# Optimization experiments

Hardware: AMD Instinct MI355X
Metric: run time of the kernel (lower is better)

The kernel has to match this reference:

```python
import jax, jax.numpy as jnp
import numpy as np

B = 1024      # batch
DIN = 103     # generator/encoder input dim
L1, L2 = 64, 32   # encoder layer widths (latent = 32)
E = 8         # NUM_EXPERTS
GH = 64       # gating hidden width
H = 256       # generator hidden width
DOUT = 51     # generator output dim
EPS = 1e-5    # BatchNorm eps


def setup_inputs() -> dict:
    key = jax.random.key(0)
    ks = jax.random.split(key, 24)
    s = 0.05
    f32 = jnp.float32
    return {
        "x": jax.random.normal(ks[0], (B, DIN), f32),
        # encoder Linear + BN params
        "w1": jax.random.normal(ks[1], (L1, DIN), f32) * s,
        "b1": jnp.zeros((L1,), f32),
        "gamma1": jnp.ones((L1,), f32),
        "beta1": jnp.zeros((L1,), f32),
        "w2": jax.random.normal(ks[2], (L2, L1), f32) * s,
        "b2": jnp.zeros((L2,), f32),
        "gamma2": jnp.ones((L2,), f32),
        "beta2": jnp.zeros((L2,), f32),
        # gating MLP (latent 32 -> GH -> GH -> E, ELU, softmax)
        "gw1": jax.random.normal(ks[3], (GH, L2), f32) * s,
        "gb1": jnp.zeros((GH,), f32),
        "gw2": jax.random.normal(ks[4], (GH, GH), f32) * s,
        "gb2": jnp.zeros((GH,), f32),
        "gw3": jax.random.normal(ks[5], (E, GH), f32) * s,
        "gb3": jnp.zeros((E,), f32),
        # expert weight banks for 3-layer generator (MANN style)
        "ew1": jax.random.normal(ks[6], (E, DIN, H), f32) * s,
        "eb1": jnp.zeros((E, H), f32),
        "ew2": jax.random.normal(ks[7], (E, H, H), f32) * s,
        "eb2": jnp.zeros((E, H), f32),
        "ew3": jax.random.normal(ks[8], (E, H, DOUT), f32) * s,
        "eb3": jnp.zeros((E, DOUT), f32),
    }


def _batchnorm(h, gamma, beta):
    # training-mode BatchNorm1d: per-batch mean/var (biased var, matching torch)
    m = jnp.mean(h, axis=0)
    v = jnp.mean((h - m) ** 2, axis=0)
    return gamma * (h - m) * jax.lax.rsqrt(v + EPS) + beta


def reference(x, w1, b1, gamma1, beta1, w2, b2, gamma2, beta2,
              gw1, gb1, gw2, gb2, gw3, gb3,
              ew1, eb1, ew2, eb2, ew3, eb3):
    # in-place scale of last 3 features (x[:,100:103] *= 100)
    xs = x.at[:, 100:103].multiply(100.0)
    # encoder: Linear -> BN -> ReLU, twice
    h = jax.nn.relu(_batchnorm(xs @ w1.T + b1, gamma1, beta1))
    latent = jax.nn.relu(_batchnorm(h @ w2.T + b2, gamma2, beta2))
    # gating network -> blending coefficients BC [B, E]
    g = jax.nn.elu(latent @ gw1.T + gb1)
    g = jax.nn.elu(g @ gw2.T + gb2)
    bc = jax.nn.softmax(g @ gw3.T + gb3, axis=-1)
    # MANN-style generator: per-sample expert-blended weights
    wb1 = jnp.einsum('be,eih->bih', bc, ew1)   # [B, DIN, H]
    h1 = jax.nn.elu(jnp.einsum('bi,bih->bh', xs, wb1) + bc @ eb1)
    wb2 = jnp.einsum('be,ehk->bhk', bc, ew2)   # [B, H, H]
    h2 = jax.nn.elu(jnp.einsum('bh,bhk->bk', h1, wb2) + bc @ eb2)
    wb3 = jnp.einsum('be,eho->bho', bc, ew3)   # [B, H, DOUT]
    out = jnp.einsum('bh,bho->bo', h2, wb3) + bc @ eb3
    return out
```

## Files before the change

### kernel.cpp

```cpp
#include <hip/hip_runtime.h>
#include <math.h>


#define DIN 103
#define NE  8
#define HH  256
#define DOUT 51
#define EPSBN 1e-5f

typedef __attribute__((ext_vector_type(8))) short bf16x8;
typedef __attribute__((ext_vector_type(4))) float f32x4;
typedef __attribute__((ext_vector_type(8))) unsigned short us8;
typedef unsigned short ushort_t;

__device__ __forceinline__ float eluf(float v) { return v > 0.f ? v : (expf(v) - 1.f); }
__device__ __forceinline__ unsigned short bf16h(float f) {
  unsigned u = __float_as_uint(f);
  u += 0x7FFFu + ((u >> 16) & 1u);
  return (unsigned short)(u >> 16);
}
__device__ __forceinline__ float bf16f(unsigned short h) { return __uint_as_float(((unsigned)h) << 16); }
__device__ __forceinline__ void split_bf16(float v, unsigned short& h, unsigned short& l) {
  h = bf16h(v);
  l = bf16h(v - bf16f(h));
}
#define MFMA __builtin_amdgcn_mfma_f32_16x16x32_bf16

#define O_SLOTS1 0
#define O_SLOTS2 8192
#define O_BCG    12288
#define O_H1RAW  20480
#define O_H2RAW  86016
#define O_XSH    118784
#define O_XSL    184320
#define O_W1H    249856
#define O_W1L    253952
#define O_E1H    258048
#define O_E1L    389120
#define O_E2H    520192
#define O_E3H    782336
#define O_A1H    847872
#define O_A1L    978944
#define O_A2H    1110016
#define O_A2L    1241088
#define O_P      1372160

__global__ __launch_bounds__(256) void k_prep(
    const float* __restrict__ x, const float* __restrict__ w1,
    const float* __restrict__ ew1, const float* __restrict__ ew2, const float* __restrict__ ew3,
    float* __restrict__ ws) {
  __shared__ float tile[32][65];
  int bk = blockIdx.x, t = threadIdx.x;
  int l2 = t & 63, c = l2 & 15, q = l2 >> 4;

  if (bk < 256) {
    int nh = bk & 3, kc = (bk >> 2) & 7, e = bk >> 5;
    int k0 = kc * 32, n0 = nh * 64;
#pragma unroll
    for (int i = 0; i < 8; ++i) {
      int kl = (t >> 6) + i * 4;
      tile[kl][t & 63] = ew2[((size_t)e * HH + k0 + kl) * HH + n0 + (t & 63)];
    }
    __syncthreads();
    int nsl = t >> 6;
    us8 H8;
#pragma unroll
    for (int j = 0; j < 8; ++j) H8[j] = bf16h(tile[q * 8 + j][nsl * 16 + c]);
    size_t dst = (((size_t)(e * 16 + nh * 4 + nsl)) * 8 + kc) * 512 + l2 * 8;
    *(us8*)((ushort_t*)(ws + O_E2H) + dst) = H8;
  } else if (bk < 384) {
    int b2 = bk - 256;
    int nh = b2 & 3, kc = (b2 >> 2) & 3, e = b2 >> 4;
    int k0 = kc * 32, n0 = nh * 64;
#pragma unroll
    for (int i = 0; i < 8; ++i) {
      int kl = (t >> 6) + i * 4;
      int k = k0 + kl;
      tile[kl][t & 63] = (k < DIN) ? ew1[((size_t)e * DIN + k) * HH + n0 + (t & 63)] : 0.f;
    }
    __syncthreads();
    int nsl = t >> 6;
    us8 H8, L8;
#pragma unroll
    for (int j = 0; j < 8; ++j) {
      unsigned short h, lo; split_bf16(tile[q * 8 + j][nsl * 16 + c], h, lo);
      H8[j] = h; L8[j] = lo;
    }
    size_t dst = (((size_t)(e * 16 + nh * 4 + nsl)) * 4 + kc) * 512 + l2 * 8;
    *(us8*)((ushort_t*)(ws + O_E1H) + dst) = H8;
    *(us8*)((ushort_t*)(ws + O_E1L) + dst) = L8;
  } else if (bk < 448) {
    int b2 = bk - 384;
    int kc = b2 & 7, e = b2 >> 3;
    int k0 = kc * 32;
#pragma unroll
    for (int i = 0; i < 8; ++i) {
      int kl = (t >> 6) + i * 4;
      int n = t & 63;
      tile[kl][n] = (n < DOUT) ? ew3[((size_t)e * HH + k0 + kl) * DOUT + n] : 0.f;
    }
    __syncthreads();
    int nsl = t >> 6;
    us8 H8;
#pragma unroll
    for (int j = 0; j < 8; ++j) H8[j] = bf16h(tile[q * 8 + j][nsl * 16 + c]);
    size_t dst = (((size_t)(e * 4 + nsl)) * 8 + kc) * 512 + l2 * 8;
    *(us8*)((ushort_t*)(ws + O_E3H) + dst) = H8;
  } else if (bk < 452) {
    int kc = bk - 448;
    int k0 = kc * 32;
    __shared__ float tw[64][33];
#pragma unroll
    for (int p8 = 0; p8 < 8; ++p8) {
      int j = (t >> 5) + p8 * 8;
      int kl = t & 31;
      int k = k0 + kl;
      tw[j][kl] = (k < DIN) ? w1[(size_t)j * DIN + k] : 0.f;
    }
    __syncthreads();
    int nsl = t >> 6;
    us8 H8, L8;
#pragma unroll
    for (int j = 0; j < 8; ++j) {
      unsigned short h, lo; split_bf16(tw[nsl * 16 + c][q * 8 + j], h, lo);
      H8[j] = h; L8[j] = lo;
    }
    size_t dst = ((size_t)nsl * 4 + kc) * 512 + l2 * 8;
    *(us8*)((ushort_t*)(ws + O_W1H) + dst) = H8;
    *(us8*)((ushort_t*)(ws + O_W1L) + dst) = L8;
  } else {
    int msub = bk - 452;
    __shared__ float xt[16][104];
    for (int i = t; i < 16 * 104; i += 256) {
      int b = i / 104, k = i - b * 104;
      float v = 0.f;
      if (k < DIN) { v = x[(size_t)(msub * 16 + b) * DIN + k]; if (k >= 100) v *= 100.f; }
      xt[b][k] = v;
    }
    __syncthreads();
    int kc = t >> 6;
    int m = c;
    us8 H8, L8;
#pragma unroll
    for (int j = 0; j < 8; ++j) {
      int k = kc * 32 + q * 8 + j;
      float v = (k < 104) ? xt[m][k] : 0.f;
      unsigned short h, lo; split_bf16(v, h, lo);
      H8[j] = h; L8[j] = lo;
    }
    size_t dst = ((size_t)msub * 4 + kc) * 512 + l2 * 8;
    *(us8*)((ushort_t*)(ws + O_XSH) + dst) = H8;
    *(us8*)((ushort_t*)(ws + O_XSL) + dst) = L8;
  }
}

__global__ __launch_bounds__(256) void k_enc1(const float* __restrict__ b1, float* __restrict__ ws) {
  __shared__ float tile[16][65];
  int bk = blockIdx.x, t = threadIdx.x;
  int wv = t >> 6, l = t & 63, c = l & 15, quad = l >> 4;
  const ushort_t* XsH = (const ushort_t*)(ws + O_XSH);
  const ushort_t* XsL = (const ushort_t*)(ws + O_XSL);
  const ushort_t* W1H = (const ushort_t*)(ws + O_W1H);
  const ushort_t* W1L = (const ushort_t*)(ws + O_W1L);
  float* h1raw  = ws + O_H1RAW;
  float* slots1 = ws + O_SLOTS1;
  f32x4 acc = {0.f, 0.f, 0.f, 0.f};
#pragma unroll
  for (int kc = 0; kc < 4; ++kc) {
    bf16x8 ah = *(const bf16x8*)(XsH + ((size_t)bk * 4 + kc) * 512 + l * 8);
    bf16x8 al = *(const bf16x8*)(XsL + ((size_t)bk * 4 + kc) * 512 + l * 8);
    bf16x8 bh = *(const bf16x8*)(W1H + ((size_t)wv * 4 + kc) * 512 + l * 8);
    bf16x8 bl = *(const bf16x8*)(W1L + ((size_t)wv * 4 + kc) * 512 + l * 8);
    acc = MFMA(ah, bh, acc, 0, 0, 0);
    acc = MFMA(al, bh, acc, 0, 0, 0);
    acc = MFMA(ah, bl, acc, 0, 0, 0);
  }
  int col = wv * 16 + c;
  float b1v = b1[col];
#pragma unroll
  for (int r = 0; r < 4; ++r) {
    float v = acc[r] + b1v;
    tile[quad * 4 + r][col] = v;
    h1raw[(size_t)(bk * 16 + quad * 4 + r) * 64 + col] = v;
  }
  __syncthreads();
  if (t < 64) {
    float s = 0.f, qq = 0.f;
    for (int r = 0; r < 16; ++r) { float v = tile[r][t]; s += v; qq += v * v; }
    slots1[bk * 128 + t] = s;
    slots1[bk * 128 + 64 + t] = qq;
  }
}

__global__ __launch_bounds__(256) void k_enc2(
    const float* __restrict__ gamma1, const float* __restrict__ beta1,
    const float* __restrict__ w2, const float* __restrict__ b2, float* __restrict__ ws) {
  __shared__ float w2T[64 * 33];
  __shared__ float red[128];
  __shared__ float sc1[64], sh1[64];
  __shared__ float h1b[16][64];
  __shared__ float hb2[16][32];
  float* slots1 = ws + O_SLOTS1;
  float* slots2 = ws + O_SLOTS2;
  float* h1raw  = ws + O_H1RAW;
  float* h2raw  = ws + O_H2RAW;
  int bk = blockIdx.x, t = threadIdx.x;
  int R0 = bk * 16;
  for (int i = t; i < 2048; i += 256) { int j = i >> 6, k = i & 63; w2T[k * 33 + j] = w2[i]; }
  if (t < 128) {
    float s = 0.f;
    for (int b = 0; b < 64; ++b) s += slots1[b * 128 + t];
    red[t] = s;
  }
  __syncthreads();
  if (t < 64) {
    float m = red[t] * (1.f / 1024.f);
    float v = red[64 + t] * (1.f / 1024.f) - m * m;
    float sc = gamma1[t] * rsqrtf(v + EPSBN);
    sc1[t] = sc; sh1[t] = beta1[t] - m * sc;
  }
  __syncthreads();
#pragma unroll
  for (int i = 0; i < 4; ++i) {
    int idx = t + i * 256;
    int r = idx >> 6, k = idx & 63;
    h1b[r][k] = fmaxf(fmaf(h1raw[(size_t)(R0 + r) * 64 + k], sc1[k], sh1[k]), 0.f);
  }
  __syncthreads();
#pragma unroll
  for (int i = 0; i < 2; ++i) {
    int o = t + i * 256;
    int r = o >> 5, j = o & 31;
    float acc = b2[j];
    for (int k = 0; k < 64; ++k) acc = fmaf(h1b[r][k], w2T[k * 33 + j], acc);
    hb2[r][j] = acc;
    h2raw[(size_t)(R0 + r) * 32 + j] = acc;
  }
  __syncthreads();
  if (t < 32) {
    float s = 0.f, q = 0.f;
    for (int r = 0; r < 16; ++r) { float v = hb2[r][t]; s += v; q += v * v; }
    slots2[bk * 64 + t] = s;
    slots2[bk * 64 + 32 + t] = q;
  }
}

__global__ __launch_bounds__(256) void k_gate(
    const float* __restrict__ gamma2, const float* __restrict__ beta2,
    const float* __restrict__ gw1, const float* __restrict__ gb1,
    const float* __restrict__ gw2, const float* __restrict__ gb2,
    const float* __restrict__ gw3, const float* __restrict__ gb3,
    float* __restrict__ ws) {
  __shared__ float red2[64], sc2[32], sh2[32];
  __shared__ float lat[16][32];
  __shared__ float gw1L[64 * 33], gw2L[64 * 65], gw3L[8 * 65];
  __shared__ float gb1L[64], gb2L[64], gb3L[8];
  __shared__ float g1[16][64], g2[16][64];
  float* slots2 = ws + O_SLOTS2;
  float* bcg    = ws + O_BCG;
  float* h2raw  = ws + O_H2RAW;
  int bk = blockIdx.x, t = threadIdx.x;
  int wv = t >> 6, l = t & 63;
  int R0 = bk * 16;
  for (int i = t; i < 2048; i += 256) { int j = i >> 5, k = i & 31; gw1L[j * 33 + k] = gw1[i]; }
  for (int i = t; i < 4096; i += 256) { int j = i >> 6, k = i & 63; gw2L[j * 65 + k] = gw2[i]; }
  for (int i = t; i < 512; i += 256) { int j = i >> 6, k = i & 63; gw3L[j * 65 + k] = gw3[i]; }
  if (t < 64) { gb1L[t] = gb1[t]; gb2L[t] = gb2[t]; }
  if (t < 8) gb3L[t] = gb3[t];
  if (t < 64) {
    float s = 0.f;
    for (int b = 0; b < 64; ++b) s += slots2[b * 64 + t];
    red2[t] = s;
  }
  __syncthreads();
  if (t < 32) {
    float m = red2[t] * (1.f / 1024.f);
    float v = red2[32 + t] * (1.f / 1024.f) - m * m;
    float sc = gamma2[t] * rsqrtf(v + EPSBN);
    sc2[t] = sc; sh2[t] = beta2[t] - m * sc;
  }
  __syncthreads();
#pragma unroll
  for (int i = 0; i < 2; ++i) {
    int idx = t + i * 256;
    int r = idx >> 5, cc = idx & 31;
    lat[r][cc] = fmaxf(fmaf(h2raw[(size_t)(R0 + r) * 32 + cc], sc2[cc], sh2[cc]), 0.f);
  }
  __syncthreads();
#pragma unroll
  for (int rr = 0; rr < 4; ++rr) {
    int r = wv * 4 + rr;
    float a1 = gb1L[l];
    for (int k = 0; k < 32; ++k) a1 = fmaf(gw1L[l * 33 + k], lat[r][k], a1);
    g1[r][l] = eluf(a1);
  }
  __syncthreads();
#pragma unroll
  for (int rr = 0; rr < 4; ++rr) {
    int r = wv * 4 + rr;
    float a2 = gb2L[l];
    for (int k = 0; k < 64; ++k) a2 = fmaf(gw2L[l * 65 + k], g1[r][k], a2);
    g2[r][l] = eluf(a2);
  }
  __syncthreads();
#pragma unroll
  for (int rr = 0; rr < 4; ++rr) {
    int r = wv * 4 + rr;
    if (l < 8) {
      float a3 = gb3L[l];
      for (int k = 0; k < 64; ++k) a3 = fmaf(gw3L[l * 65 + k], g2[r][k], a3);
      float mx = a3;
      mx = fmaxf(mx, __shfl_xor(mx, 1));
      mx = fmaxf(mx, __shfl_xor(mx, 2));
      mx = fmaxf(mx, __shfl_xor(mx, 4));
      float p = expf(a3 - mx);
      float sp = p;
      sp += __shfl_xor(sp, 1); sp += __shfl_xor(sp, 2); sp += __shfl_xor(sp, 4);
      bcg[(size_t)(R0 + r) * 8 + l] = p / sp;
    }
  }
}

__global__ __launch_bounds__(256) void k_gen1(float* __restrict__ ws) {
  int bk = blockIdx.x, e = blockIdx.y, t = threadIdx.x;
  int wv = t >> 6, l = t & 63, c = l & 15, quad = l >> 4;
  const ushort_t* XsH = (const ushort_t*)(ws + O_XSH);
  const ushort_t* XsL = (const ushort_t*)(ws + O_XSL);
  const ushort_t* E1H = (const ushort_t*)(ws + O_E1H);
  const ushort_t* E1L = (const ushort_t*)(ws + O_E1L);
  float* p = ws + O_P;
  f32x4 acc[4] = {};
#pragma unroll
  for (int kc = 0; kc < 4; ++kc) {
    bf16x8 ah = *(const bf16x8*)(XsH + ((size_t)bk * 4 + kc) * 512 + l * 8);
    bf16x8 al = *(const bf16x8*)(XsL + ((size_t)bk * 4 + kc) * 512 + l * 8);
#pragma unroll
    for (int nsi = 0; nsi < 4; ++nsi) {
      int ns = wv * 4 + nsi;
      size_t bo = (((size_t)(e * 16 + ns)) * 4 + kc) * 512 + l * 8;
      bf16x8 bh = *(const bf16x8*)(E1H + bo);
      bf16x8 bl = *(const bf16x8*)(E1L + bo);
      acc[nsi] = MFMA(ah, bh, acc[nsi], 0, 0, 0);
      acc[nsi] = MFMA(al, bh, acc[nsi], 0, 0, 0);
      acc[nsi] = MFMA(ah, bl, acc[nsi], 0, 0, 0);
    }
  }
  float* pe = p + (size_t)e * 262144;
#pragma unroll
  for (int nsi = 0; nsi < 4; ++nsi) {
    int col = (wv * 4 + nsi) * 16 + c;
#pragma unroll
    for (int r = 0; r < 4; ++r)
      pe[(size_t)(bk * 16 + quad * 4 + r) * 256 + col] = acc[nsi][r];
  }
}

__global__ __launch_bounds__(256) void k_gen2(float* __restrict__ ws) {
  int bk = blockIdx.x, e = blockIdx.y, t = threadIdx.x;
  int wv = t >> 6, l = t & 63, c = l & 15, quad = l >> 4;
  const ushort_t* AH = (const ushort_t*)(ws + O_A1H);
  const ushort_t* AL = (const ushort_t*)(ws + O_A1L);
  const ushort_t* E2H = (const ushort_t*)(ws + O_E2H);
  float* p = ws + O_P;
  f32x4 acc[4] = {};
#pragma unroll
  for (int kc = 0; kc < 8; ++kc) {
    bf16x8 ah = *(const bf16x8*)(AH + ((size_t)bk * 8 + kc) * 512 + l * 8);
    bf16x8 al = *(const bf16x8*)(AL + ((size_t)bk * 8 + kc) * 512 + l * 8);
#pragma unroll
    for (int nsi = 0; nsi < 4; ++nsi) {
      int ns = wv * 4 + nsi;
      size_t bo = (((size_t)(e * 16 + ns)) * 8 + kc) * 512 + l * 8;
      bf16x8 bh = *(const bf16x8*)(E2H + bo);
      acc[nsi] = MFMA(ah, bh, acc[nsi], 0, 0, 0);
      acc[nsi] = MFMA(al, bh, acc[nsi], 0, 0, 0);
    }
  }
  float* pe = p + (size_t)e * 262144;
#pragma unroll
  for (int nsi = 0; nsi < 4; ++nsi) {
    int col = (wv * 4 + nsi) * 16 + c;
#pragma unroll
    for (int r = 0; r < 4; ++r)
      pe[(size_t)(bk * 16 + quad * 4 + r) * 256 + col] = acc[nsi][r];
  }
}

__global__ __launch_bounds__(256) void k_gen3(float* __restrict__ ws) {
  int bk = blockIdx.x, eg = blockIdx.y, t = threadIdx.x;
  int wv = t >> 6, l = t & 63, c = l & 15, quad = l >> 4;
  int e = eg * 4 + wv;
  const ushort_t* AH = (const ushort_t*)(ws + O_A2H);
  const ushort_t* AL = (const ushort_t*)(ws + O_A2L);
  const ushort_t* E3H = (const ushort_t*)(ws + O_E3H);
  float* p3 = ws + O_P;
  f32x4 acc[4] = {};
#pragma unroll
  for (int kc = 0; kc < 8; ++kc) {
    bf16x8 ah = *(const bf16x8*)(AH + ((size_t)bk * 8 + kc) * 512 + l * 8);
    bf16x8 al = *(const bf16x8*)(AL + ((size_t)bk * 8 + kc) * 512 + l * 8);
#pragma unroll
    for (int nsi = 0; nsi < 4; ++nsi) {
      size_t bo = (((size_t)(e * 4 + nsi)) * 8 + kc) * 512 + l * 8;
      bf16x8 bh = *(const bf16x8*)(E3H + bo);
      acc[nsi] = MFMA(ah, bh, acc[nsi], 0, 0, 0);
      acc[nsi] = MFMA(al, bh, acc[nsi], 0, 0, 0);
    }
  }
  float* pe = p3 + (size_t)e * 65536;
#pragma unroll
  for (int nsi = 0; nsi < 4; ++nsi) {
    int col = nsi * 16 + c;
#pragma unroll
    for (int r = 0; r < 4; ++r)
      pe[(size_t)(bk * 16 + quad * 4 + r) * 64 + col] = acc[nsi][r];
  }
}

__global__ __launch_bounds__(256) void k_comb(const float* __restrict__ eb,
    float* __restrict__ ws, int dstH, int dstL) {
  int gid = blockIdx.x * 256 + threadIdx.x;
  int l2 = gid & 63, kc = (gid >> 6) & 7, msub = gid >> 9;
  int b = msub * 16 + (l2 & 15);
  int k0 = kc * 32 + (l2 >> 4) * 8;
  const float* p = ws + O_P;
  const float* bc = ws + O_BCG;
  unsigned short* ah = (unsigned short*)(ws + dstH);
  unsigned short* al = (unsigned short*)(ws + dstL);
  float wv[NE];
#pragma unroll
  for (int e = 0; e < NE; ++e) wv[e] = bc[b * NE + e];
  float s[8] = {};
#pragma unroll
  for (int e = 0; e < NE; ++e) {
    const float* pr = p + (size_t)e * 262144 + (size_t)b * HH + k0;
    float4 p0 = *(const float4*)pr, p1 = *(const float4*)(pr + 4);
    const float* er = eb + e * HH + k0;
    float4 e0 = *(const float4*)er, e1 = *(const float4*)(er + 4);
    s[0] = fmaf(wv[e], p0.x + e0.x, s[0]);
    s[1] = fmaf(wv[e], p0.y + e0.y, s[1]);
    s[2] = fmaf(wv[e], p0.z + e0.z, s[2]);
    s[3] = fmaf(wv[e], p0.w + e0.w, s[3]);
    s[4] = fmaf(wv[e], p1.x + e1.x, s[4]);
    s[5] = fmaf(wv[e], p1.y + e1.y, s[5]);
    s[6] = fmaf(wv[e], p1.z + e1.z, s[6]);
    s[7] = fmaf(wv[e], p1.w + e1.w, s[7]);
  }
  us8 H, L;
#pragma unroll
  for (int j = 0; j < 8; ++j) {
    float v = eluf(s[j]);
    unsigned short h, lo; split_bf16(v, h, lo);
    H[j] = h; L[j] = lo;
  }
  *(us8*)(ah + (size_t)gid * 8) = H;
  *(us8*)(al + (size_t)gid * 8) = L;
}

__global__ __launch_bounds__(256) void k_comb3(const float* __restrict__ eb3,
    float* __restrict__ ws, float* __restrict__ out) {
  int gid = blockIdx.x * 256 + threadIdx.x;
  int b = gid >> 6, o = gid & 63;
  if (o >= DOUT) return;
  const float* p3 = ws + O_P;
  const float* bc = ws + O_BCG;
  float s = 0.f;
#pragma unroll
  for (int e = 0; e < NE; ++e)
    s = fmaf(bc[b * NE + e], p3[(size_t)e * 65536 + (size_t)b * 64 + o] + eb3[e * DOUT + o], s);
  out[(size_t)b * DOUT + o] = s;
}

extern "C" void kernel_launch(void* const* d_in, const int* in_sizes, int n_in,
                              void* d_out, int out_size, void* d_ws, size_t ws_size,
                              hipStream_t stream) {
  const float* x      = (const float*)d_in[0];
  const float* w1     = (const float*)d_in[1];
  const float* b1     = (const float*)d_in[2];
  const float* gamma1 = (const float*)d_in[3];
  const float* beta1  = (const float*)d_in[4];
  const float* w2     = (const float*)d_in[5];
  const float* b2     = (const float*)d_in[6];
  const float* gamma2 = (const float*)d_in[7];
  const float* beta2  = (const float*)d_in[8];
  const float* gw1    = (const float*)d_in[9];
  const float* gb1    = (const float*)d_in[10];
  const float* gw2    = (const float*)d_in[11];
  const float* gb2    = (const float*)d_in[12];
  const float* gw3    = (const float*)d_in[13];
  const float* gb3    = (const float*)d_in[14];
  const float* ew1    = (const float*)d_in[15];
  const float* eb1    = (const float*)d_in[16];
  const float* ew2    = (const float*)d_in[17];
  const float* eb2    = (const float*)d_in[18];
  const float* ew3    = (const float*)d_in[19];
  const float* eb3    = (const float*)d_in[20];
  float* wsf  = (float*)d_ws;
  float* outp = (float*)d_out;

  k_prep<<<516, 256, 0, stream>>>(x, w1, ew1, ew2, ew3, wsf);
  k_enc1<<<64, 256, 0, stream>>>(b1, wsf);
  k_enc2<<<64, 256, 0, stream>>>(gamma1, beta1, w2, b2, wsf);
  k_gate<<<64, 256, 0, stream>>>(gamma2, beta2, gw1, gb1, gw2, gb2, gw3, gb3, wsf);
  k_gen1<<<dim3(64, 8), 256, 0, stream>>>(wsf);
  k_comb<<<128, 256, 0, stream>>>(eb1, wsf, O_A1H, O_A1L);
  k_gen2<<<dim3(64, 8), 256, 0, stream>>>(wsf);
  k_comb<<<128, 256, 0, stream>>>(eb2, wsf, O_A2H, O_A2L);
  k_gen3<<<dim3(64, 2), 256, 0, stream>>>(wsf);
  k_comb3<<<256, 256, 0, stream>>>(eb3, wsf, outp);
}
```

Before: 160.1 us.

## Merge independent kernels to cut launches and fuse gen3 with final combine

Merges k_prep with enc1, computing the first encoder layer in plain FP32 from shared memory instead of the MFMA path with split bf16. Runs gen1 and the gating network as disjoint block ranges of a single launch, since they do not depend on each other. Fuses gen3 and comb3 into one 512-thread kernel that keeps per-expert partials in shared memory rather than writing them to global memory. This takes the launch count from 10 to 7 and removes one global round trip, at the cost of larger blocks and a slower scalar enc1.

```diff
diff --git a/kernel.cpp b/kernel.cpp
--- a/kernel.cpp
+++ b/kernel.cpp
@@ -33,8 +33,6 @@
 #define O_H2RAW  86016
 #define O_XSH    118784
 #define O_XSL    184320
-#define O_W1H    249856
-#define O_W1L    253952
 #define O_E1H    258048
 #define O_E1L    389120
 #define O_E2H    520192
@@ -45,11 +43,15 @@
 #define O_A2L    1241088
 #define O_P      1372160
 
-__global__ __launch_bounds__(256) void k_prep(
-    const float* __restrict__ x, const float* __restrict__ w1,
+__global__ __launch_bounds__(256) void k_prep_enc1(
+    const float* __restrict__ x, const float* __restrict__ w1, const float* __restrict__ b1,
     const float* __restrict__ ew1, const float* __restrict__ ew2, const float* __restrict__ ew3,
     float* __restrict__ ws) {
-  __shared__ float tile[32][65];
+  __shared__ union {
+    float tile[32][65];
+    float xt[16][104];
+    struct { float w1L[64 * DIN]; float xr[16][104]; float hb[16][64]; } e1;
+  } sm;
   int bk = blockIdx.x, t = threadIdx.x;
   int l2 = t & 63, c = l2 & 15, q = l2 >> 4;
 
@@ -59,13 +61,13 @@
 #pragma unroll
     for (int i = 0; i < 8; ++i) {
       int kl = (t >> 6) + i * 4;
-      tile[kl][t & 63] = ew2[((size_t)e * HH + k0 + kl) * HH + n0 + (t & 63)];
+      sm.tile[kl][t & 63] = ew2[((size_t)e * HH + k0 + kl) * HH + n0 + (t & 63)];
     }
     __syncthreads();
     int nsl = t >> 6;
     us8 H8;
 #pragma unroll
-    for (int j = 0; j < 8; ++j) H8[j] = bf16h(tile[q * 8 + j][nsl * 16 + c]);
+    for (int j = 0; j < 8; ++j) H8[j] = bf16h(sm.tile[q * 8 + j][nsl * 16 + c]);
     size_t dst = (((size_t)(e * 16 + nh * 4 + nsl)) * 8 + kc) * 512 + l2 * 8;
     *(us8*)((ushort_t*)(ws + O_E2H) + dst) = H8;
   } else if (bk < 384) {
@@ -76,14 +78,14 @@
     for (int i = 0; i < 8; ++i) {
       int kl = (t >> 6) + i * 4;
       int k = k0 + kl;
-      tile[kl][t & 63] = (k < DIN) ? ew1[((size_t)e * DIN + k) * HH + n0 + (t & 63)] : 0.f;
+      sm.tile[kl][t & 63] = (k < DIN) ? ew1[((size_t)e * DIN + k) * HH + n0 + (t & 63)] : 0.f;
     }
     __syncthreads();
     int nsl = t >> 6;
     us8 H8, L8;
 #pragma unroll
     for (int j = 0; j < 8; ++j) {
-      unsigned short h, lo; split_bf16(tile[q * 8 + j][nsl * 16 + c], h, lo);
+      unsigned short h, lo; split_bf16(sm.tile[q * 8 + j][nsl * 16 + c], h, lo);
       H8[j] = h; L8[j] = lo;
     }
     size_t dst = (((size_t)(e * 16 + nh * 4 + nsl)) * 4 + kc) * 512 + l2 * 8;
@@ -97,45 +99,22 @@
     for (int i = 0; i < 8; ++i) {
       int kl = (t >> 6) + i * 4;
       int n = t & 63;
-      tile[kl][n] = (n < DOUT) ? ew3[((size_t)e * HH + k0 + kl) * DOUT + n] : 0.f;
+      sm.tile[kl][n] = (n < DOUT) ? ew3[((size_t)e * HH + k0 + kl) * DOUT + n] : 0.f;
     }
     __syncthreads();
     int nsl = t >> 6;
     us8 H8;
 #pragma unroll
-    for (int j = 0; j < 8; ++j) H8[j] = bf16h(tile[q * 8 + j][nsl * 16 + c]);
+    for (int j = 0; j < 8; ++j) H8[j] = bf16h(sm.tile[q * 8 + j][nsl * 16 + c]);
     size_t dst = (((size_t)(e * 4 + nsl)) * 8 + kc) * 512 + l2 * 8;
     *(us8*)((ushort_t*)(ws + O_E3H) + dst) = H8;
-  } else if (bk < 452) {
-    int kc = bk - 448;
-    int k0 = kc * 32;
-    __shared__ float tw[64][33];
-#pragma unroll
-    for (int p8 = 0; p8 < 8; ++p8) {
-      int j = (t >> 5) + p8 * 8;
-      int kl = t & 31;
-      int k = k0 + kl;
-      tw[j][kl] = (k < DIN) ? w1[(size_t)j * DIN + k] : 0.f;
-    }
-    __syncthreads();
-    int nsl = t >> 6;
-    us8 H8, L8;
-#pragma unroll
-    for (int j = 0; j < 8; ++j) {
-      unsigned short h, lo; split_bf16(tw[nsl * 16 + c][q * 8 + j], h, lo);
-      H8[j] = h; L8[j] = lo;
-    }
-    size_t dst = ((size_t)nsl * 4 + kc) * 512 + l2 * 8;
-    *(us8*)((ushort_t*)(ws + O_W1H) + dst) = H8;
-    *(us8*)((ushort_t*)(ws + O_W1L) + dst) = L8;
-  } else {
-    int msub = bk - 452;
-    __shared__ float xt[16][104];
+  } else if (bk < 512) {
+    int msub = bk - 448;
     for (int i = t; i < 16 * 104; i += 256) {
       int b = i / 104, k = i - b * 104;
       float v = 0.f;
       if (k < DIN) { v = x[(size_t)(msub * 16 + b) * DIN + k]; if (k >= 100) v *= 100.f; }
-      xt[b][k] = v;
+      sm.xt[b][k] = v;
     }
     __syncthreads();
     int kc = t >> 6;
@@ -144,51 +123,42 @@
 #pragma unroll
     for (int j = 0; j < 8; ++j) {
       int k = kc * 32 + q * 8 + j;
-      float v = (k < 104) ? xt[m][k] : 0.f;
+      float v = (k < 104) ? sm.xt[m][k] : 0.f;
       unsigned short h, lo; split_bf16(v, h, lo);
       H8[j] = h; L8[j] = lo;
     }
     size_t dst = ((size_t)msub * 4 + kc) * 512 + l2 * 8;
     *(us8*)((ushort_t*)(ws + O_XSH) + dst) = H8;
     *(us8*)((ushort_t*)(ws + O_XSL) + dst) = L8;
-  }
-}
-
-__global__ __launch_bounds__(256) void k_enc1(const float* __restrict__ b1, float* __restrict__ ws) {
-  __shared__ float tile[16][65];
-  int bk = blockIdx.x, t = threadIdx.x;
-  int wv = t >> 6, l = t & 63, c = l & 15, quad = l >> 4;
-  const ushort_t* XsH = (const ushort_t*)(ws + O_XSH);
-  const ushort_t* XsL = (const ushort_t*)(ws + O_XSL);
-  const ushort_t* W1H = (const ushort_t*)(ws + O_W1H);
-  const ushort_t* W1L = (const ushort_t*)(ws + O_W1L);
-  float* h1raw  = ws + O_H1RAW;
-  float* slots1 = ws + O_SLOTS1;
-  f32x4 acc = {0.f, 0.f, 0.f, 0.f};
-#pragma unroll
-  for (int kc = 0; kc < 4; ++kc) {
-    bf16x8 ah = *(const bf16x8*)(XsH + ((size_t)bk * 4 + kc) * 512 + l * 8);
-    bf16x8 al = *(const bf16x8*)(XsL + ((size_t)bk * 4 + kc) * 512 + l * 8);
-    bf16x8 bh = *(const bf16x8*)(W1H + ((size_t)wv * 4 + kc) * 512 + l * 8);
-    bf16x8 bl = *(const bf16x8*)(W1L + ((size_t)wv * 4 + kc) * 512 + l * 8);
-    acc = MFMA(ah, bh, acc, 0, 0, 0);
-    acc = MFMA(al, bh, acc, 0, 0, 0);
-    acc = MFMA(ah, bl, acc, 0, 0, 0);
-  }
-  int col = wv * 16 + c;
-  float b1v = b1[col];
-#pragma unroll
-  for (int r = 0; r < 4; ++r) {
-    float v = acc[r] + b1v;
-    tile[quad * 4 + r][col] = v;
-    h1raw[(size_t)(bk * 16 + quad * 4 + r) * 64 + col] = v;
-  }
-  __syncthreads();
-  if (t < 64) {
-    float s = 0.f, qq = 0.f;
-    for (int r = 0; r < 16; ++r) { float v = tile[r][t]; s += v; qq += v * v; }
-    slots1[bk * 128 + t] = s;
-    slots1[bk * 128 + 64 + t] = qq;
+  } else {
+    float* slots1 = ws + O_SLOTS1;
+    float* h1raw  = ws + O_H1RAW;
+    int bkl = bk - 512;
+    int r0 = bkl * 16;
+    for (int i = t; i < 64 * DIN; i += 256) sm.e1.w1L[i] = w1[i];
+    for (int i = t; i < 16 * 104; i += 256) {
+      int r = i / 104, c2 = i - r * 104;
+      float v = 0.f;
+      if (c2 < DIN) { v = x[(size_t)(r0 + r) * DIN + c2]; if (c2 >= 100) v *= 100.f; }
+      sm.e1.xr[r][c2] = v;
+    }
+    __syncthreads();
+#pragma unroll
+    for (int i = 0; i < 4; ++i) {
+      int idx = t + i * 256;
+      int r = idx >> 6, j = idx & 63;
+      float acc = b1[j];
+      for (int k = 0; k < DIN; ++k) acc = fmaf(sm.e1.xr[r][k], sm.e1.w1L[j * DIN + k], acc);
+      sm.e1.hb[r][j] = acc;
+      h1raw[(size_t)(r0 + r) * 64 + j] = acc;
+    }
+    __syncthreads();
+    if (t < 64) {
+      float s = 0.f, qq = 0.f;
+      for (int r = 0; r < 16; ++r) { float v = sm.e1.hb[r][t]; s += v; qq += v * v; }
+      slots1[bkl * 128 + t] = s;
+      slots1[bkl * 128 + 64 + t] = qq;
+    }
   }
 }
 
@@ -245,113 +215,114 @@
   }
 }
 
-__global__ __launch_bounds__(256) void k_gate(
+__global__ __launch_bounds__(256) void k_gen1_gate(
     const float* __restrict__ gamma2, const float* __restrict__ beta2,
     const float* __restrict__ gw1, const float* __restrict__ gb1,
     const float* __restrict__ gw2, const float* __restrict__ gb2,
     const float* __restrict__ gw3, const float* __restrict__ gb3,
     float* __restrict__ ws) {
-  __shared__ float red2[64], sc2[32], sh2[32];
-  __shared__ float lat[16][32];
-  __shared__ float gw1L[64 * 33], gw2L[64 * 65], gw3L[8 * 65];
-  __shared__ float gb1L[64], gb2L[64], gb3L[8];
-  __shared__ float g1[16][64], g2[16][64];
-  float* slots2 = ws + O_SLOTS2;
-  float* bcg    = ws + O_BCG;
-  float* h2raw  = ws + O_H2RAW;
-  int bk = blockIdx.x, t = threadIdx.x;
+  int blk = blockIdx.x, t = threadIdx.x;
   int wv = t >> 6, l = t & 63;
-  int R0 = bk * 16;
-  for (int i = t; i < 2048; i += 256) { int j = i >> 5, k = i & 31; gw1L[j * 33 + k] = gw1[i]; }
-  for (int i = t; i < 4096; i += 256) { int j = i >> 6, k = i & 63; gw2L[j * 65 + k] = gw2[i]; }
-  for (int i = t; i < 512; i += 256) { int j = i >> 6, k = i & 63; gw3L[j * 65 + k] = gw3[i]; }
-  if (t < 64) { gb1L[t] = gb1[t]; gb2L[t] = gb2[t]; }
-  if (t < 8) gb3L[t] = gb3[t];
-  if (t < 64) {
-    float s = 0.f;
-    for (int b = 0; b < 64; ++b) s += slots2[b * 64 + t];
-    red2[t] = s;
-  }
-  __syncthreads();
-  if (t < 32) {
-    float m = red2[t] * (1.f / 1024.f);
-    float v = red2[32 + t] * (1.f / 1024.f) - m * m;
-    float sc = gamma2[t] * rsqrtf(v + EPSBN);
-    sc2[t] = sc; sh2[t] = beta2[t] - m * sc;
-  }
-  __syncthreads();
-#pragma unroll
-  for (int i = 0; i < 2; ++i) {
-    int idx = t + i * 256;
-    int r = idx >> 5, cc = idx & 31;
-    lat[r][cc] = fmaxf(fmaf(h2raw[(size_t)(R0 + r) * 32 + cc], sc2[cc], sh2[cc]), 0.f);
-  }
-  __syncthreads();
-#pragma unroll
-  for (int rr = 0; rr < 4; ++rr) {
-    int r = wv * 4 + rr;
-    float a1 = gb1L[l];
-    for (int k = 0; k < 32; ++k) a1 = fmaf(gw1L[l * 33 + k], lat[r][k], a1);
-    g1[r][l] = eluf(a1);
-  }
-  __syncthreads();
-#pragma unroll
-  for (int rr = 0; rr < 4; ++rr) {
-    int r = wv * 4 + rr;
-    float a2 = gb2L[l];
-    for (int k = 0; k < 64; ++k) a2 = fmaf(gw2L[l * 65 + k], g1[r][k], a2);
-    g2[r][l] = eluf(a2);
-  }
-  __syncthreads();
-#pragma unroll
-  for (int rr = 0; rr < 4; ++rr) {
-    int r = wv * 4 + rr;
-    if (l < 8) {
-      float a3 = gb3L[l];
-      for (int k = 0; k < 64; ++k) a3 = fmaf(gw3L[l * 65 + k], g2[r][k], a3);
-      float mx = a3;
-      mx = fmaxf(mx, __shfl_xor(mx, 1));
-      mx = fmaxf(mx, __shfl_xor(mx, 2));
-      mx = fmaxf(mx, __shfl_xor(mx, 4));
-      float p = expf(a3 - mx);
-      float sp = p;
-      sp += __shfl_xor(sp, 1); sp += __shfl_xor(sp, 2); sp += __shfl_xor(sp, 4);
-      bcg[(size_t)(R0 + r) * 8 + l] = p / sp;
-    }
-  }
-}
-
-__global__ __launch_bounds__(256) void k_gen1(float* __restrict__ ws) {
-  int bk = blockIdx.x, e = blockIdx.y, t = threadIdx.x;
-  int wv = t >> 6, l = t & 63, c = l & 15, quad = l >> 4;
-  const ushort_t* XsH = (const ushort_t*)(ws + O_XSH);
-  const ushort_t* XsL = (const ushort_t*)(ws + O_XSL);
-  const ushort_t* E1H = (const ushort_t*)(ws + O_E1H);
-  const ushort_t* E1L = (const ushort_t*)(ws + O_E1L);
-  float* p = ws + O_P;
-  f32x4 acc[4] = {};
-#pragma unroll
-  for (int kc = 0; kc < 4; ++kc) {
-    bf16x8 ah = *(const bf16x8*)(XsH + ((size_t)bk * 4 + kc) * 512 + l * 8);
-    bf16x8 al = *(const bf16x8*)(XsL + ((size_t)bk * 4 + kc) * 512 + l * 8);
+  if (blk < 512) {
+    int bk = blk >> 3, e = blk & 7;
+    int c = l & 15, quad = l >> 4;
+    const ushort_t* XsH = (const ushort_t*)(ws + O_XSH);
+    const ushort_t* XsL = (const ushort_t*)(ws + O_XSL);
+    const ushort_t* E1H = (const ushort_t*)(ws + O_E1H);
+    const ushort_t* E1L = (const ushort_t*)(ws + O_E1L);
+    float* p = ws + O_P;
+    f32x4 acc[4] = {};
+#pragma unroll
+    for (int kc = 0; kc < 4; ++kc) {
+      bf16x8 ah = *(const bf16x8*)(XsH + ((size_t)bk * 4 + kc) * 512 + l * 8);
+      bf16x8 al = *(const bf16x8*)(XsL + ((size_t)bk * 4 + kc) * 512 + l * 8);
+#pragma unroll
+      for (int nsi = 0; nsi < 4; ++nsi) {
+        int ns = wv * 4 + nsi;
+        size_t bo = (((size_t)(e * 16 + ns)) * 4 + kc) * 512 + l * 8;
+        bf16x8 bh = *(const bf16x8*)(E1H + bo);
+        bf16x8 bl = *(const bf16x8*)(E1L + bo);
+        acc[nsi] = MFMA(ah, bh, acc[nsi], 0, 0, 0);
+        acc[nsi] = MFMA(al, bh, acc[nsi], 0, 0, 0);
+        acc[nsi] = MFMA(ah, bl, acc[nsi], 0, 0, 0);
+      }
+    }
+    float* pe = p + (size_t)e * 262144;
 #pragma unroll
     for (int nsi = 0; nsi < 4; ++nsi) {
-      int ns = wv * 4 + nsi;
-      size_t bo = (((size_t)(e * 16 + ns)) * 4 + kc) * 512 + l * 8;
-      bf16x8 bh = *(const bf16x8*)(E1H + bo);
-      bf16x8 bl = *(const bf16x8*)(E1L + bo);
-      acc[nsi] = MFMA(ah, bh, acc[nsi], 0, 0, 0);
-      acc[nsi] = MFMA(al, bh, acc[nsi], 0, 0, 0);
-      acc[nsi] = MFMA(ah, bl, acc[nsi], 0, 0, 0);
-    }
-  }
-  float* pe = p + (size_t)e * 262144;
-#pragma unroll
-  for (int nsi = 0; nsi < 4; ++nsi) {
-    int col = (wv * 4 + nsi) * 16 + c;
-#pragma unroll
-    for (int r = 0; r < 4; ++r)
-      pe[(size_t)(bk * 16 + quad * 4 + r) * 256 + col] = acc[nsi][r];
+      int col = (wv * 4 + nsi) * 16 + c;
+#pragma unroll
+      for (int r = 0; r < 4; ++r)
+        pe[(size_t)(bk * 16 + quad * 4 + r) * 256 + col] = acc[nsi][r];
+    }
+  } else {
+    __shared__ float red2[64], sc2[32], sh2[32];
+    __shared__ float lat[16][32];
+    __shared__ float gw1L[64 * 33], gw2L[64 * 65], gw3L[8 * 65];
+    __shared__ float gb1L[64], gb2L[64], gb3L[8];
+    __shared__ float g1[16][64], g2[16][64];
+    float* slots2 = ws + O_SLOTS2;
+    float* bcg    = ws + O_BCG;
+    float* h2raw  = ws + O_H2RAW;
+    int bk = blk - 512;
+    int R0 = bk * 16;
+    for (int i = t; i < 2048; i += 256) { int j = i >> 5, k = i & 31; gw1L[j * 33 + k] = gw1[i]; }
+    for (int i = t; i < 4096; i += 256) { int j = i >> 6, k = i & 63; gw2L[j * 65 + k] = gw2[i]; }
+    for (int i = t; i < 512; i += 256) { int j = i >> 6, k = i & 63; gw3L[j * 65 + k] = gw3[i]; }
+    if (t < 64) { gb1L[t] = gb1[t]; gb2L[t] = gb2[t]; }
+    if (t < 8) gb3L[t] = gb3[t];
+    if (t < 64) {
+      float s = 0.f;
+      for (int b = 0; b < 64; ++b) s += slots2[b * 64 + t];
+      red2[t] = s;
+    }
+    __syncthreads();
+    if (t < 32) {
+      float m = red2[t] * (1.f / 1024.f);
+      float v = red2[32 + t] * (1.f / 1024.f) - m * m;
+      float sc = gamma2[t] * rsqrtf(v + EPSBN);
+      sc2[t] = sc; sh2[t] = beta2[t] - m * sc;
+    }
+    __syncthreads();
+#pragma unroll
+    for (int i = 0; i < 2; ++i) {
+      int idx = t + i * 256;
+      int r = idx >> 5, cc = idx & 31;
+      lat[r][cc] = fmaxf(fmaf(h2raw[(size_t)(R0 + r) * 32 + cc], sc2[cc], sh2[cc]), 0.f);
+    }
+    __syncthreads();
+#pragma unroll
+    for (int rr = 0; rr < 4; ++rr) {
+      int r = wv * 4 + rr;
+      float a1 = gb1L[l];
+      for (int k = 0; k < 32; ++k) a1 = fmaf(gw1L[l * 33 + k], lat[r][k], a1);
+      g1[r][l] = eluf(a1);
+    }
+    __syncthreads();
+#pragma unroll
+    for (int rr = 0; rr < 4; ++rr) {
+      int r = wv * 4 + rr;
+      float a2 = gb2L[l];
+      for (int k = 0; k < 64; ++k) a2 = fmaf(gw2L[l * 65 + k], g1[r][k], a2);
+      g2[r][l] = eluf(a2);
+    }
+    __syncthreads();
+#pragma unroll
+    for (int rr = 0; rr < 4; ++rr) {
+      int r = wv * 4 + rr;
+      if (l < 8) {
+        float a3 = gb3L[l];
+        for (int k = 0; k < 64; ++k) a3 = fmaf(gw3L[l * 65 + k], g2[r][k], a3);
+        float mx = a3;
+        mx = fmaxf(mx, __shfl_xor(mx, 1));
+        mx = fmaxf(mx, __shfl_xor(mx, 2));
+        mx = fmaxf(mx, __shfl_xor(mx, 4));
+        float p = expf(a3 - mx);
+        float sp = p;
+        sp += __shfl_xor(sp, 1); sp += __shfl_xor(sp, 2); sp += __shfl_xor(sp, 4);
+        bcg[(size_t)(R0 + r) * 8 + l] = p / sp;
+      }
+    }
   }
 }
 
@@ -383,37 +354,6 @@
 #pragma unroll
     for (int r = 0; r < 4; ++r)
       pe[(size_t)(bk * 16 + quad * 4 + r) * 256 + col] = acc[nsi][r];
-  }
-}
-
-__global__ __launch_bounds__(256) void k_gen3(float* __restrict__ ws) {
-  int bk = blockIdx.x, eg = blockIdx.y, t = threadIdx.x;
-  int wv = t >> 6, l = t & 63, c = l & 15, quad = l >> 4;
-  int e = eg * 4 + wv;
-  const ushort_t* AH = (const ushort_t*)(ws + O_A2H);
-  const ushort_t* AL = (const ushort_t*)(ws + O_A2L);
-  const ushort_t* E3H = (const ushort_t*)(ws + O_E3H);
-  float* p3 = ws + O_P;
-  f32x4 acc[4] = {};
-#pragma unroll
-  for (int kc = 0; kc < 8; ++kc) {
-    bf16x8 ah = *(const bf16x8*)(AH + ((size_t)bk * 8 + kc) * 512 + l * 8);
-    bf16x8 al = *(const bf16x8*)(AL + ((size_t)bk * 8 + kc) * 512 + l * 8);
-#pragma unroll
-    for (int nsi = 0; nsi < 4; ++nsi) {
-      size_t bo = (((size_t)(e * 4 + nsi)) * 8 + kc) * 512 + l * 8;
-      bf16x8 bh = *(const bf16x8*)(E3H + bo);
-      acc[nsi] = MFMA(ah, bh, acc[nsi], 0, 0, 0);
-      acc[nsi] = MFMA(al, bh, acc[nsi], 0, 0, 0);
-    }
-  }
-  float* pe = p3 + (size_t)e * 65536;
-#pragma unroll
-  for (int nsi = 0; nsi < 4; ++nsi) {
-    int col = nsi * 16 + c;
-#pragma unroll
-    for (int r = 0; r < 4; ++r)
-      pe[(size_t)(bk * 16 + quad * 4 + r) * 64 + col] = acc[nsi][r];
   }
 }
 
@@ -457,18 +397,55 @@
   *(us8*)(al + (size_t)gid * 8) = L;
 }
 
-__global__ __launch_bounds__(256) void k_comb3(const float* __restrict__ eb3,
+__global__ __launch_bounds__(512) void k_gen3c(const float* __restrict__ eb3,
     float* __restrict__ ws, float* __restrict__ out) {
-  int gid = blockIdx.x * 256 + threadIdx.x;
-  int b = gid >> 6, o = gid & 63;
-  if (o >= DOUT) return;
-  const float* p3 = ws + O_P;
-  const float* bc = ws + O_BCG;
-  float s = 0.f;
-#pragma unroll
-  for (int e = 0; e < NE; ++e)
-    s = fmaf(bc[b * NE + e], p3[(size_t)e * 65536 + (size_t)b * 64 + o] + eb3[e * DOUT + o], s);
-  out[(size_t)b * DOUT + o] = s;
+  __shared__ float p3s[8][16][64];
+  __shared__ float bcL[16][8];
+  __shared__ float eb3L[8][64];
+  int bk = blockIdx.x, t = threadIdx.x;
+  int wv = t >> 6, l = t & 63, c = l & 15, quad = l >> 4;
+  int R0 = bk * 16;
+  const ushort_t* AH = (const ushort_t*)(ws + O_A2H);
+  const ushort_t* AL = (const ushort_t*)(ws + O_A2L);
+  const ushort_t* E3H = (const ushort_t*)(ws + O_E3H);
+  const float* bcg = ws + O_BCG;
+  if (t < 128) bcL[t >> 3][t & 7] = bcg[(size_t)(R0 + (t >> 3)) * 8 + (t & 7)];
+  if (t >= 128 && t < 640 - 128) {
+  }
+  {
+    int i = t;
+    if (i < 512) { int e = i >> 6, n = i & 63; eb3L[e][n] = (n < DOUT) ? eb3[e * DOUT + n] : 0.f; }
+  }
+  int e = wv;
+  f32x4 acc[4] = {};
+#pragma unroll
+  for (int kc = 0; kc < 8; ++kc) {
+    bf16x8 ah = *(const bf16x8*)(AH + ((size_t)bk * 8 + kc) * 512 + l * 8);
+    bf16x8 al = *(const bf16x8*)(AL + ((size_t)bk * 8 + kc) * 512 + l * 8);
+#pragma unroll
+    for (int nsi = 0; nsi < 4; ++nsi) {
+      size_t bo = (((size_t)(e * 4 + nsi)) * 8 + kc) * 512 + l * 8;
+      bf16x8 bh = *(const bf16x8*)(E3H + bo);
+      acc[nsi] = MFMA(ah, bh, acc[nsi], 0, 0, 0);
+      acc[nsi] = MFMA(al, bh, acc[nsi], 0, 0, 0);
+    }
+  }
+#pragma unroll
+  for (int nsi = 0; nsi < 4; ++nsi)
+#pragma unroll
+    for (int r = 0; r < 4; ++r)
+      p3s[e][quad * 4 + r][nsi * 16 + c] = acc[nsi][r];
+  __syncthreads();
+#pragma unroll
+  for (int i = 0; i < 2; ++i) {
+    int idx = t + i * 512;
+    int row = idx >> 6, col = idx & 63;
+    float s = 0.f;
+#pragma unroll
+    for (int e2 = 0; e2 < 8; ++e2)
+      s = fmaf(bcL[row][e2], p3s[e2][row][col] + eb3L[e2][col], s);
+    if (col < DOUT) out[(size_t)(R0 + row) * DOUT + col] = s;
+  }
 }
 
 extern "C" void kernel_launch(void* const* d_in, const int* in_sizes, int n_in,
@@ -498,14 +475,11 @@
   float* wsf  = (float*)d_ws;
   float* outp = (float*)d_out;
 
-  k_prep<<<516, 256, 0, stream>>>(x, w1, ew1, ew2, ew3, wsf);
-  k_enc1<<<64, 256, 0, stream>>>(b1, wsf);
+  k_prep_enc1<<<576, 256, 0, stream>>>(x, w1, b1, ew1, ew2, ew3, wsf);
   k_enc2<<<64, 256, 0, stream>>>(gamma1, beta1, w2, b2, wsf);
-  k_gate<<<64, 256, 0, stream>>>(gamma2, beta2, gw1, gb1, gw2, gb2, gw3, gb3, wsf);
-  k_gen1<<<dim3(64, 8), 256, 0, stream>>>(wsf);
+  k_gen1_gate<<<576, 256, 0, stream>>>(gamma2, beta2, gw1, gb1, gw2, gb2, gw3, gb3, wsf);
   k_comb<<<128, 256, 0, stream>>>(eb1, wsf, O_A1H, O_A1L);
   k_gen2<<<dim3(64, 8), 256, 0, stream>>>(wsf);
   k_comb<<<128, 256, 0, stream>>>(eb2, wsf, O_A2H, O_A2L);
-  k_gen3<<<dim3(64, 2), 256, 0, stream>>>(wsf);
-  k_comb3<<<256, 256, 0, stream>>>(eb3, wsf, outp);
-}
+  k_gen3c<<<64, 512, 0, stream>>>(eb3, wsf, outp);
+}
```

Result: no change. 158.6 us (-0.9%).
